# Performance work log

Measured on AMD Instinct MI355X. Metric: run time of the kernel, lower is better.

The kernel has to match this reference:

```python
import jax, jax.numpy as jnp
import numpy as np

VOCAB, E, HIDDEN = 100000, 64, (64, 128, 64)
B, T = 4096, 200


def setup_inputs() -> dict:
    key = jax.random.key(0)
    ks = jax.random.split(key, 12)
    # glorot-ish scales
    def glorot(k, shape):
        fan_in, fan_out = shape[0], shape[-1]
        s = jnp.sqrt(6.0 / (fan_in + fan_out))
        return jax.random.uniform(k, shape, jnp.float32, -s, s)
    return {
        "query": jax.random.randint(ks[0], (B,), 0, VOCAB),
        "keys": jax.random.randint(ks[1], (B, T), 0, VOCAB),
        "emb": glorot(ks[2], (VOCAB, E)),
        "att_w1": glorot(ks[3], (4 * E, 64)),
        "att_b1": jnp.zeros((64,), jnp.float32),
        "att_w2": glorot(ks[4], (64, 1)),
        "att_b2": jnp.zeros((1,), jnp.float32),
        "deep_w1": glorot(ks[5], (HIDDEN[0], HIDDEN[1])),
        "deep_b1": jnp.zeros((HIDDEN[1],), jnp.float32),
        "deep_w2": glorot(ks[6], (HIDDEN[1], HIDDEN[2])),
        "deep_b2": jnp.zeros((HIDDEN[2],), jnp.float32),
        "out_w": glorot(ks[7], (HIDDEN[2], 1)),
        "out_b": jnp.zeros((1,), jnp.float32),
    }


def reference(query, keys, emb, att_w1, att_b1, att_w2, att_b2,
              deep_w1, deep_b1, deep_w2, deep_b2, out_w, out_b):
    q = emb[query]                # [B, E]
    k = emb[keys]                 # [B, T, E]
    qe = jnp.broadcast_to(q[:, None, :], k.shape)  # [B, T, E]
    inter = jnp.concatenate([qe, k, qe - k, qe * k], axis=-1)  # [B, T, 4E]
    h = jax.nn.relu(inter @ att_w1 + att_b1)       # [B, T, 64]
    scores = (h @ att_w2 + att_b2)[..., 0]         # [B, T]
    w = jax.nn.softmax(scores, axis=-1)            # [B, T]
    interest = jnp.einsum("bt,bte->be", w, k)      # [B, E]
    d = jax.nn.relu(interest @ deep_w1 + deep_b1)
    d = jax.nn.relu(d @ deep_w2 + deep_b2)
    return jax.nn.sigmoid(d @ out_w + out_b)       # [B, 1]
```

## Files before the change

kernel.cpp:

```cpp
#include <hip/hip_runtime.h>

#define T 200
#define E 64
#define TPAD 256
#define ROW 72
#define BDIM 256
#define TP 208

typedef __bf16 bf16_t;
typedef __bf16 bf16x8 __attribute__((ext_vector_type(8)));
typedef float f32x4 __attribute__((ext_vector_type(4)));

__global__ __launch_bounds__(256) void emb_cvt(const float* __restrict__ src,
                                               bf16_t* __restrict__ dst, int n8) {
    const int i = blockIdx.x * 256 + threadIdx.x;
    if (i >= n8) return;
    const float4* s = (const float4*)src + (size_t)i * 2;
    const float4 a = s[0], b = s[1];
    union { bf16_t h[8]; uint4 v; } u;
    u.h[0] = (bf16_t)a.x; u.h[1] = (bf16_t)a.y; u.h[2] = (bf16_t)a.z; u.h[3] = (bf16_t)a.w;
    u.h[4] = (bf16_t)b.x; u.h[5] = (bf16_t)b.y; u.h[6] = (bf16_t)b.z; u.h[7] = (bf16_t)b.w;
    ((uint4*)dst)[i] = u.v;
}

__global__ __launch_bounds__(256) void w1_cvt(const float* __restrict__ w1,
                                              float* __restrict__ Ap,
                                              float* __restrict__ Ctf,
                                              float* __restrict__ Dtf) {
    const int idx = blockIdx.x * 256 + threadIdx.x;
    const int e = idx >> 6, j = idx & 63;
    const float a = w1[e * 64 + j];
    const float b = w1[(64 + e) * 64 + j];
    const float c = w1[(128 + e) * 64 + j];
    const float d = w1[(192 + e) * 64 + j];
    Ap[e * 64 + j]  = a + c;
    Ctf[j * 64 + e] = b - c;
    Dtf[j * 64 + e] = d;
}

__global__ __launch_bounds__(256, 4) void din_fast(
    const int* __restrict__ query,
    const int* __restrict__ keys,
    const bf16_t* __restrict__ emb16,
    const float* __restrict__ Ap,
    const float* __restrict__ Ctf,
    const float* __restrict__ Dtf,
    const float* __restrict__ b1,
    const float* __restrict__ w2,
    const float* __restrict__ b2,
    const float* __restrict__ dw1,
    const float* __restrict__ db1,
    const float* __restrict__ dw2,
    const float* __restrict__ db2,
    const float* __restrict__ ow,
    const float* __restrict__ ob,
    float* __restrict__ out)
{
    __shared__ __align__(16) char smem[39936];
    bf16_t* sK   = (bf16_t*)smem;
    bf16_t* sMt  = (bf16_t*)(smem + 29952);
    float*  sUP  = (float*)(smem + 39168);
    float*  sQf  = (float*)(smem + 39680);
    float*  sWgt = (float*)(smem + 29952);
    float*  sRed = (float*)(smem + 30784);
    float*  sInt = (float*)(smem + 30816);
    float*  sD1  = (float*)(smem + 31072);
    float*  sD2  = (float*)(smem + 31584);
    float*  sIP  = (float*)(smem + 31840);

    const int tid  = threadIdx.x;
    const int lane = tid & 63;
    const int wid  = tid >> 6;
    const int b    = blockIdx.x;
    const float b2v = b2[0];

    uint4 kr[8];
    if (tid < T) {
        const int ki = keys[b * T + tid];
        const uint4* kp = (const uint4*)(emb16 + (size_t)ki * E);
        #pragma unroll
        for (int c = 0; c < 8; ++c) kr[c] = kp[c];
    } else {
        #pragma unroll
        for (int c = 0; c < 8; ++c) kr[c] = make_uint4(0u, 0u, 0u, 0u);
    }

    const int qi = query[b];
    if (tid < 64) sQf[tid] = (float)emb16[(size_t)qi * E + tid];
    __syncthreads();

    if (tid < 128) {
        const int j = tid & 63, ec = tid >> 6;
        float au = 0.f;
        #pragma unroll
        for (int eo = 0; eo < 32; ++eo) {
            const int e = ec * 32 + eo;
            au = fmaf(sQf[e], Ap[e * 64 + j], au);
        }
        sUP[tid] = au;
    }
    {
        const int j = tid & 63, h = tid >> 6;
        const float* cp = Ctf + j * 64 + h * 16;
        const float* dp = Dtf + j * 64 + h * 16;
        const float* qp = sQf + h * 16;
        bf16_t mo[16] __attribute__((aligned(16)));
        #pragma unroll
        for (int x = 0; x < 16; ++x)
            mo[x] = (bf16_t)fmaf(qp[x], dp[x], cp[x]);
        *(bf16x8*)&sMt[j * ROW + h * 16]     = *(bf16x8*)&mo[0];
        *(bf16x8*)&sMt[j * ROW + h * 16 + 8] = *(bf16x8*)&mo[8];
    }
    __syncthreads();

    if (tid < TP) {
        uint4* dst = (uint4*)(sK + tid * ROW);
        #pragma unroll
        for (int c = 0; c < 8; ++c) dst[c] = kr[c];
    }
    __syncthreads();

    {
        const int n    = lane & 15;
        const int quad = lane >> 4;
        float w2v[4], uv[4];
        bf16x8 bF[4][2];
        #pragma unroll
        for (int nt = 0; nt < 4; ++nt) {
            const int jj = nt * 16 + n;
            w2v[nt] = w2[jj];
            uv[nt]  = b1[jj] + sUP[jj] + sUP[64 + jj];
            bF[nt][0] = *(const bf16x8*)&sMt[jj * ROW + quad * 8];
            bF[nt][1] = *(const bf16x8*)&sMt[jj * ROW + 32 + quad * 8];
        }
        __syncthreads();

        for (int mt = wid; mt < 13; mt += 4) {
            const bf16x8 a0 = *(const bf16x8*)&sK[(mt * 16 + n) * ROW + quad * 8];
            const bf16x8 a1 = *(const bf16x8*)&sK[(mt * 16 + n) * ROW + 32 + quad * 8];
            float s0 = 0.f, s1 = 0.f, s2 = 0.f, s3 = 0.f;
            #pragma unroll
            for (int nt = 0; nt < 4; ++nt) {
                f32x4 acc = { uv[nt], uv[nt], uv[nt], uv[nt] };
                acc = __builtin_amdgcn_mfma_f32_16x16x32_bf16(a0, bF[nt][0], acc, 0, 0, 0);
                acc = __builtin_amdgcn_mfma_f32_16x16x32_bf16(a1, bF[nt][1], acc, 0, 0, 0);
                s0 = fmaf(fmaxf(acc[0], 0.f), w2v[nt], s0);
                s1 = fmaf(fmaxf(acc[1], 0.f), w2v[nt], s1);
                s2 = fmaf(fmaxf(acc[2], 0.f), w2v[nt], s2);
                s3 = fmaf(fmaxf(acc[3], 0.f), w2v[nt], s3);
            }
            #pragma unroll
            for (int off = 1; off < 16; off <<= 1) {
                s0 += __shfl_xor(s0, off);
                s1 += __shfl_xor(s1, off);
                s2 += __shfl_xor(s2, off);
                s3 += __shfl_xor(s3, off);
            }
            if (n == 0) {
                const int base = mt * 16 + quad * 4;
                sWgt[base + 0] = s0;
                sWgt[base + 1] = s1;
                sWgt[base + 2] = s2;
                sWgt[base + 3] = s3;
            }
        }
    }
    __syncthreads();

    {
        const float score = (tid < T) ? (sWgt[tid] + b2v) : -1e30f;
        float m = score;
        #pragma unroll
        for (int off = 32; off > 0; off >>= 1) m = fmaxf(m, __shfl_xor(m, off));
        if (lane == 0) sRed[wid] = m;
        __syncthreads();
        const float gmax = fmaxf(fmaxf(sRed[0], sRed[1]), fmaxf(sRed[2], sRed[3]));
        const float p = (tid < T) ? __expf(score - gmax) : 0.f;
        float s = p;
        #pragma unroll
        for (int off = 32; off > 0; off >>= 1) s += __shfl_xor(s, off);
        if (lane == 0) sRed[4 + wid] = s;
        __syncthreads();
        const float gsum = sRed[4] + sRed[5] + sRed[6] + sRed[7];
        if (tid < T) sWgt[tid] = p / gsum;
    }
    __syncthreads();

    {
        const int e = tid & 63, ch = tid >> 6;
        float a = 0.f;
        #pragma unroll 10
        for (int tt = 0; tt < 50; ++tt) {
            const int t = ch * 50 + tt;
            a = fmaf(sWgt[t], (float)sK[t * ROW + e], a);
        }
        sIP[tid] = a;
    }
    __syncthreads();
    if (tid < 64) sInt[tid] = sIP[tid] + sIP[64 + tid] + sIP[128 + tid] + sIP[192 + tid];
    __syncthreads();

    if (tid < 128) {
        float a = db1[tid];
        #pragma unroll 8
        for (int e = 0; e < 64; ++e) a = fmaf(sInt[e], dw1[e * 128 + tid], a);
        sD1[tid] = fmaxf(a, 0.f);
    }
    __syncthreads();
    if (tid < 64) {
        float a = db2[tid];
        #pragma unroll 8
        for (int i = 0; i < 128; ++i) a = fmaf(sD1[i], dw2[i * 64 + tid], a);
        sD2[tid] = fmaxf(a, 0.f);
    }
    __syncthreads();
    if (tid < 64) {
        float v = sD2[tid] * ow[tid];
        #pragma unroll
        for (int off = 32; off > 0; off >>= 1) v += __shfl_xor(v, off);
        if (tid == 0) out[b] = 1.f / (1.f + __expf(-(v + ob[0])));
    }
}

__global__ __launch_bounds__(BDIM, 3) void din_kernel(
    const int* __restrict__ query,
    const int* __restrict__ keys,
    const float* __restrict__ embf,
    const bf16_t* __restrict__ emb16,
    const int use16,
    const float* __restrict__ w1,
    const float* __restrict__ b1,
    const float* __restrict__ w2,
    const float* __restrict__ b2,
    const float* __restrict__ dw1,
    const float* __restrict__ db1,
    const float* __restrict__ dw2,
    const float* __restrict__ db2,
    const float* __restrict__ ow,
    const float* __restrict__ ob,
    float* __restrict__ out)
{
    __shared__ __align__(16) char sRaw[TPAD * ROW * 2];
    __shared__ __align__(16) bf16_t sMt[64 * ROW];
    __shared__ float sU[64];
    __shared__ float sUP[256];
    __shared__ float sW2f[64];
    __shared__ float sWgt[256];
    __shared__ float sQf[64];
    __shared__ __align__(16) char sQtmp[128];
    __shared__ float sRed[8];
    __shared__ float sInt[64];
    __shared__ float sD1[128];
    __shared__ float sD2[64];

    const int tid  = threadIdx.x;
    const int lane = tid & 63;
    const int wid  = tid >> 6;
    const int b    = blockIdx.x;
    const float b2v = b2[0];

    uint4 kr[8];
    if (tid < T) {
        const int ki = keys[b * T + tid];
        if (use16) {
            const uint4* kp = (const uint4*)(emb16 + (size_t)ki * E);
            #pragma unroll
            for (int c = 0; c < 8; ++c) kr[c] = kp[c];
        } else {
            const float4* kp = (const float4*)(embf + (size_t)ki * E);
            #pragma unroll
            for (int c = 0; c < 8; ++c) {
                const float4 x = kp[2 * c], y = kp[2 * c + 1];
                union { bf16_t h[8]; uint4 v; } u;
                u.h[0] = (bf16_t)x.x; u.h[1] = (bf16_t)x.y; u.h[2] = (bf16_t)x.z; u.h[3] = (bf16_t)x.w;
                u.h[4] = (bf16_t)y.x; u.h[5] = (bf16_t)y.y; u.h[6] = (bf16_t)y.z; u.h[7] = (bf16_t)y.w;
                kr[c] = u.v;
            }
        }
    } else {
        #pragma unroll
        for (int c = 0; c < 8; ++c) kr[c] = make_uint4(0u, 0u, 0u, 0u);
    }

    const int qi = query[b];
    if (tid < 8) {
        uint4 qv;
        if (use16) {
            qv = ((const uint4*)(emb16 + (size_t)qi * E))[tid];
        } else {
            const float4 x = ((const float4*)(embf + (size_t)qi * E))[2 * tid];
            const float4 y = ((const float4*)(embf + (size_t)qi * E))[2 * tid + 1];
            union { bf16_t h[8]; uint4 v; } u;
            u.h[0] = (bf16_t)x.x; u.h[1] = (bf16_t)x.y; u.h[2] = (bf16_t)x.z; u.h[3] = (bf16_t)x.w;
            u.h[4] = (bf16_t)y.x; u.h[5] = (bf16_t)y.y; u.h[6] = (bf16_t)y.z; u.h[7] = (bf16_t)y.w;
            qv = u.v;
        }
        ((uint4*)sQtmp)[tid] = qv;
    }
    if (tid < 64) sW2f[tid] = w2[tid];
    __syncthreads();
    if (tid < 64) sQf[tid] = (float)((const bf16_t*)sQtmp)[tid];
    __syncthreads();

    {
        float* sTmp = (float*)sRaw;
        const int j = tid & 63, ec = tid >> 6;
        float au = 0.f;
        #pragma unroll
        for (int eo = 0; eo < 16; ++eo) {
            const int e = ec * 16 + eo;
            const float w1a = w1[e * 64 + j];
            const float w1b = w1[(64 + e) * 64 + j];
            const float w1c = w1[(128 + e) * 64 + j];
            const float w1d = w1[(192 + e) * 64 + j];
            sTmp[e * 65 + j] = w1b - w1c + sQf[e] * w1d;
            au = fmaf(sQf[e], w1a + w1c, au);
        }
        sUP[tid] = au;
    }
    __syncthreads();
    {
        const float* sTmp = (const float*)sRaw;
        const int e = tid & 63, jc = tid >> 6;
        #pragma unroll
        for (int jo = 0; jo < 16; ++jo) {
            const int j = jc * 16 + jo;
            sMt[j * ROW + e] = (bf16_t)sTmp[e * 65 + j];
        }
    }
    if (tid < 64) sU[tid] = b1[tid] + sUP[tid] + sUP[64 + tid] + sUP[128 + tid] + sUP[192 + tid];
    __syncthreads();

    bf16_t* sK = (bf16_t*)sRaw;
    {
        uint4* dst = (uint4*)(sK + tid * ROW);
        #pragma unroll
        for (int c = 0; c < 8; ++c) dst[c] = kr[c];
    }
    __syncthreads();

    {
        const int n    = lane & 15;
        const int quad = lane >> 4;
        float w2v[4], uv[4];
        bf16x8 bF[4][2];
        #pragma unroll
        for (int nt = 0; nt < 4; ++nt) {
            w2v[nt] = sW2f[nt * 16 + n];
            uv[nt]  = sU[nt * 16 + n];
            bF[nt][0] = *(const bf16x8*)&sMt[(nt * 16 + n) * ROW + quad * 8];
            bF[nt][1] = *(const bf16x8*)&sMt[(nt * 16 + n) * ROW + 32 + quad * 8];
        }
        #pragma unroll
        for (int i = 0; i < 4; ++i) {
            const int mt = wid * 4 + i;
            const bf16x8 a0 = *(const bf16x8*)&sK[(mt * 16 + n) * ROW + quad * 8];
            const bf16x8 a1 = *(const bf16x8*)&sK[(mt * 16 + n) * ROW + 32 + quad * 8];
            float s0 = 0.f, s1 = 0.f, s2 = 0.f, s3 = 0.f;
            #pragma unroll
            for (int nt = 0; nt < 4; ++nt) {
                f32x4 acc = { uv[nt], uv[nt], uv[nt], uv[nt] };
                acc = __builtin_amdgcn_mfma_f32_16x16x32_bf16(a0, bF[nt][0], acc, 0, 0, 0);
                acc = __builtin_amdgcn_mfma_f32_16x16x32_bf16(a1, bF[nt][1], acc, 0, 0, 0);
                s0 = fmaf(fmaxf(acc[0], 0.f), w2v[nt], s0);
                s1 = fmaf(fmaxf(acc[1], 0.f), w2v[nt], s1);
                s2 = fmaf(fmaxf(acc[2], 0.f), w2v[nt], s2);
                s3 = fmaf(fmaxf(acc[3], 0.f), w2v[nt], s3);
            }
            #pragma unroll
            for (int off = 1; off < 16; off <<= 1) {
                s0 += __shfl_xor(s0, off);
                s1 += __shfl_xor(s1, off);
                s2 += __shfl_xor(s2, off);
                s3 += __shfl_xor(s3, off);
            }
            if (n == 0) {
                const int base = mt * 16 + quad * 4;
                sWgt[base + 0] = s0;
                sWgt[base + 1] = s1;
                sWgt[base + 2] = s2;
                sWgt[base + 3] = s3;
            }
        }
    }
    __syncthreads();

    {
        const float score = (tid < T) ? (sWgt[tid] + b2v) : -1e30f;
        float m = score;
        #pragma unroll
        for (int off = 32; off > 0; off >>= 1) m = fmaxf(m, __shfl_xor(m, off));
        if (lane == 0) sRed[wid] = m;
        __syncthreads();
        const float gmax = fmaxf(fmaxf(sRed[0], sRed[1]), fmaxf(sRed[2], sRed[3]));
        const float p = (tid < T) ? __expf(score - gmax) : 0.f;
        float s = p;
        #pragma unroll
        for (int off = 32; off > 0; off >>= 1) s += __shfl_xor(s, off);
        if (lane == 0) sRed[4 + wid] = s;
        __syncthreads();
        const float gsum = sRed[4] + sRed[5] + sRed[6] + sRed[7];
        sWgt[tid] = p / gsum;
    }
    __syncthreads();

    {
        const int e = tid & 63, ch = tid >> 6;
        float a = 0.f;
        #pragma unroll 8
        for (int tt = 0; tt < 64; ++tt) {
            const int t = ch * 64 + tt;
            a = fmaf(sWgt[t], (float)sK[t * ROW + e], a);
        }
        sUP[tid] = a;
    }
    __syncthreads();
    if (tid < 64) sInt[tid] = sUP[tid] + sUP[64 + tid] + sUP[128 + tid] + sUP[192 + tid];
    __syncthreads();

    if (tid < 128) {
        float a = db1[tid];
        #pragma unroll 8
        for (int e = 0; e < 64; ++e) a = fmaf(sInt[e], dw1[e * 128 + tid], a);
        sD1[tid] = fmaxf(a, 0.f);
    }
    __syncthreads();
    if (tid < 64) {
        float a = db2[tid];
        #pragma unroll 8
        for (int i = 0; i < 128; ++i) a = fmaf(sD1[i], dw2[i * 64 + tid], a);
        sD2[tid] = fmaxf(a, 0.f);
    }
    __syncthreads();
    if (tid < 64) {
        float v = sD2[tid] * ow[tid];
        #pragma unroll
        for (int off = 32; off > 0; off >>= 1) v += __shfl_xor(v, off);
        if (tid == 0) out[b] = 1.f / (1.f + __expf(-(v + ob[0])));
    }
}

extern "C" void kernel_launch(void* const* d_in, const int* in_sizes, int n_in,
                              void* d_out, int out_size, void* d_ws, size_t ws_size,
                              hipStream_t stream) {
    const int*   query = (const int*)d_in[0];
    const int*   keys  = (const int*)d_in[1];
    const float* embf  = (const float*)d_in[2];
    const float* w1    = (const float*)d_in[3];
    const float* b1    = (const float*)d_in[4];
    const float* w2    = (const float*)d_in[5];
    const float* b2    = (const float*)d_in[6];
    const float* dw1   = (const float*)d_in[7];
    const float* db1   = (const float*)d_in[8];
    const float* dw2   = (const float*)d_in[9];
    const float* db2   = (const float*)d_in[10];
    const float* ow    = (const float*)d_in[11];
    const float* ob    = (const float*)d_in[12];
    float* out = (float*)d_out;
    const int B        = in_sizes[0];
    const int embElems = in_sizes[2];
    const size_t WOFF  = 49152;

    if (ws_size >= WOFF + (size_t)embElems * 2) {
        float*  Ap    = (float*)d_ws;
        float*  Ctf   = (float*)((char*)d_ws + 16384);
        float*  Dtf   = (float*)((char*)d_ws + 32768);
        bf16_t* emb16 = (bf16_t*)((char*)d_ws + WOFF);
        const int n8 = embElems / 8;
        w1_cvt<<<16, 256, 0, stream>>>(w1, Ap, Ctf, Dtf);
        emb_cvt<<<(n8 + 255) / 256, 256, 0, stream>>>(embf, emb16, n8);
        din_fast<<<B, BDIM, 0, stream>>>(query, keys, emb16, Ap, Ctf, Dtf,
                                         b1, w2, b2, dw1, db1, dw2, db2, ow, ob, out);
    } else {
        const int use16 = (ws_size >= (size_t)embElems * 2) ? 1 : 0;
        bf16_t* emb16 = (bf16_t*)d_ws;
        if (use16) {
            const int n8 = embElems / 8;
            emb_cvt<<<(n8 + 255) / 256, 256, 0, stream>>>(embf, emb16, n8);
        }
        din_kernel<<<B, BDIM, 0, stream>>>(query, keys, embf, emb16, use16,
                                           w1, b1, w2, b2, dw1, db1, dw2, db2, ow, ob, out);
    }
}
```

Baseline: 163.4 us.

## Shrink LDS with XOR-swizzled unpadded rows to raise occupancy to six blocks

Replaces the padded 72-element row layout with 128-byte rows using an XOR swizzle to avoid bank conflicts. The M matrix and the key tile now share the same region, reusing buffers so LDS drops from about 39.9KB to 27.2KB. Launch bounds go from 4 to 6 blocks per CU. The weighted-sum stage uses 128 threads over 100 timesteps each, which removes one reduction barrier. The swizzled layout leaves padded rows 200-207 uninitialised for the 13th MFMA tile; those scores are masked later, but the register cap of 6 blocks per CU may cause spills.

```diff
diff --git a/kernel.cpp b/kernel.cpp
--- a/kernel.cpp
+++ b/kernel.cpp
@@ -5,7 +5,6 @@
 #define TPAD 256
 #define ROW 72
 #define BDIM 256
-#define TP 208
 
 typedef __bf16 bf16_t;
 typedef __bf16 bf16x8 __attribute__((ext_vector_type(8)));
@@ -38,7 +37,7 @@
     Dtf[j * 64 + e] = d;
 }
 
-__global__ __launch_bounds__(256, 4) void din_fast(
+__global__ __launch_bounds__(256, 6) void din_fast(
     const int* __restrict__ query,
     const int* __restrict__ keys,
     const bf16_t* __restrict__ emb16,
@@ -56,17 +55,14 @@
     const float* __restrict__ ob,
     float* __restrict__ out)
 {
-    __shared__ __align__(16) char smem[39936];
-    bf16_t* sK   = (bf16_t*)smem;
-    bf16_t* sMt  = (bf16_t*)(smem + 29952);
-    float*  sUP  = (float*)(smem + 39168);
-    float*  sQf  = (float*)(smem + 39680);
-    float*  sWgt = (float*)(smem + 29952);
-    float*  sRed = (float*)(smem + 30784);
-    float*  sInt = (float*)(smem + 30816);
-    float*  sD1  = (float*)(smem + 31072);
-    float*  sD2  = (float*)(smem + 31584);
-    float*  sIP  = (float*)(smem + 31840);
+    __shared__ __align__(16) char smem[27232];
+    float* sWgt = (float*)(smem + 25600);
+    float* sRed = (float*)(smem + 26432);
+    float* sIP  = (float*)(smem + 26464);
+    float* sQf  = (float*)(smem + 26976);
+    float* sUP  = (float*)(smem + 25600);
+    float* sD1  = (float*)(smem + 25600);
+    float* sD2  = (float*)(smem + 26112);
 
     const int tid  = threadIdx.x;
     const int lane = tid & 63;
@@ -80,27 +76,25 @@
         const uint4* kp = (const uint4*)(emb16 + (size_t)ki * E);
         #pragma unroll
         for (int c = 0; c < 8; ++c) kr[c] = kp[c];
-    } else {
-        #pragma unroll
-        for (int c = 0; c < 8; ++c) kr[c] = make_uint4(0u, 0u, 0u, 0u);
     }
 
     const int qi = query[b];
     if (tid < 64) sQf[tid] = (float)emb16[(size_t)qi * E + tid];
     __syncthreads();
 
+    const int j = tid & 63;
+    const int h = tid >> 6;
+
     if (tid < 128) {
-        const int j = tid & 63, ec = tid >> 6;
         float au = 0.f;
         #pragma unroll
         for (int eo = 0; eo < 32; ++eo) {
-            const int e = ec * 32 + eo;
+            const int e = h * 32 + eo;
             au = fmaf(sQf[e], Ap[e * 64 + j], au);
         }
         sUP[tid] = au;
     }
     {
-        const int j = tid & 63, h = tid >> 6;
         const float* cp = Ctf + j * 64 + h * 16;
         const float* dp = Dtf + j * 64 + h * 16;
         const float* qp = sQf + h * 16;
@@ -108,36 +102,44 @@
         #pragma unroll
         for (int x = 0; x < 16; ++x)
             mo[x] = (bf16_t)fmaf(qp[x], dp[x], cp[x]);
-        *(bf16x8*)&sMt[j * ROW + h * 16]     = *(bf16x8*)&mo[0];
-        *(bf16x8*)&sMt[j * ROW + h * 16 + 8] = *(bf16x8*)&mo[8];
-    }
-    __syncthreads();
-
-    if (tid < TP) {
-        uint4* dst = (uint4*)(sK + tid * ROW);
-        #pragma unroll
-        for (int c = 0; c < 8; ++c) dst[c] = kr[c];
-    }
-    __syncthreads();
-
-    {
-        const int n    = lane & 15;
-        const int quad = lane >> 4;
-        float w2v[4], uv[4];
-        bf16x8 bF[4][2];
-        #pragma unroll
-        for (int nt = 0; nt < 4; ++nt) {
-            const int jj = nt * 16 + n;
-            w2v[nt] = w2[jj];
-            uv[nt]  = b1[jj] + sUP[jj] + sUP[64 + jj];
-            bF[nt][0] = *(const bf16x8*)&sMt[jj * ROW + quad * 8];
-            bF[nt][1] = *(const bf16x8*)&sMt[jj * ROW + 32 + quad * 8];
-        }
-        __syncthreads();
-
+        char* rowp = smem + j * 128;
+        const int rx = (j & 7) << 4;
+        *(uint4*)(rowp + ((h * 32) ^ rx))      = *(uint4*)&mo[0];
+        *(uint4*)(rowp + ((h * 32 + 16) ^ rx)) = *(uint4*)&mo[8];
+    }
+    __syncthreads();
+
+    const int n    = lane & 15;
+    const int quad = lane >> 4;
+    float w2v[4], uv[4];
+    bf16x8 bF[4][2];
+    #pragma unroll
+    for (int nt = 0; nt < 4; ++nt) {
+        const int jj = nt * 16 + n;
+        w2v[nt] = w2[jj];
+        uv[nt]  = b1[jj] + sUP[jj] + sUP[64 + jj];
+        const char* rp = smem + jj * 128;
+        const int rxj = (jj & 7) << 4;
+        bF[nt][0] = *(const bf16x8*)(rp + ((quad * 16) ^ rxj));
+        bF[nt][1] = *(const bf16x8*)(rp + ((64 + quad * 16) ^ rxj));
+    }
+    __syncthreads();
+
+    if (tid < T) {
+        char* rowp = smem + tid * 128;
+        const int rx = (tid & 7) << 4;
+        #pragma unroll
+        for (int c = 0; c < 8; ++c)
+            *(uint4*)(rowp + ((c * 16) ^ rx)) = kr[c];
+    }
+    __syncthreads();
+
+    {
+        const int rxn = (n & 7) << 4;
         for (int mt = wid; mt < 13; mt += 4) {
-            const bf16x8 a0 = *(const bf16x8*)&sK[(mt * 16 + n) * ROW + quad * 8];
-            const bf16x8 a1 = *(const bf16x8*)&sK[(mt * 16 + n) * ROW + 32 + quad * 8];
+            const char* rp = smem + (mt * 16 + n) * 128;
+            const bf16x8 a0 = *(const bf16x8*)(rp + ((quad * 16) ^ rxn));
+            const bf16x8 a1 = *(const bf16x8*)(rp + ((64 + quad * 16) ^ rxn));
             float s0 = 0.f, s1 = 0.f, s2 = 0.f, s3 = 0.f;
             #pragma unroll
             for (int nt = 0; nt < 4; ++nt) {
@@ -186,24 +188,24 @@
     }
     __syncthreads();
 
-    {
+    if (tid < 128) {
         const int e = tid & 63, ch = tid >> 6;
         float a = 0.f;
         #pragma unroll 10
-        for (int tt = 0; tt < 50; ++tt) {
-            const int t = ch * 50 + tt;
-            a = fmaf(sWgt[t], (float)sK[t * ROW + e], a);
+        for (int tt = 0; tt < 100; ++tt) {
+            const int t = ch * 100 + tt;
+            const bf16_t kv = *(const bf16_t*)(smem + t * 128 + ((e * 2) ^ ((t & 7) << 4)));
+            a = fmaf(sWgt[t], (float)kv, a);
         }
         sIP[tid] = a;
     }
-    __syncthreads();
-    if (tid < 64) sInt[tid] = sIP[tid] + sIP[64 + tid] + sIP[128 + tid] + sIP[192 + tid];
     __syncthreads();
 
     if (tid < 128) {
         float a = db1[tid];
         #pragma unroll 8
-        for (int e = 0; e < 64; ++e) a = fmaf(sInt[e], dw1[e * 128 + tid], a);
+        for (int e = 0; e < 64; ++e)
+            a = fmaf(sIP[e] + sIP[64 + e], dw1[e * 128 + tid], a);
         sD1[tid] = fmaxf(a, 0.f);
     }
     __syncthreads();
```

Measured after the change: 220.1 us. 1.35x slower.

## Merge preprocessing kernels and coalesce key-embedding gather across 8-thread groups

Applied to the files above, without the earlier changes.

Merges the weight-transform and embedding-conversion kernels into one launch, saving one kernel launch and the gap between launches. Changes the key-row gather so each group of 8 threads loads one 128-byte embedding row with each thread taking one 16-byte chunk, instead of one thread loading a whole row. This should give coalesced global loads and fewer outstanding loads per thread. The fallback path no longer builds a bf16 copy and always uses the fp32 embedding table.

```diff
diff --git a/kernel.cpp b/kernel.cpp
--- a/kernel.cpp
+++ b/kernel.cpp
@@ -11,31 +11,33 @@
 typedef __bf16 bf16x8 __attribute__((ext_vector_type(8)));
 typedef float f32x4 __attribute__((ext_vector_type(4)));
 
-__global__ __launch_bounds__(256) void emb_cvt(const float* __restrict__ src,
-                                               bf16_t* __restrict__ dst, int n8) {
-    const int i = blockIdx.x * 256 + threadIdx.x;
+__global__ __launch_bounds__(256) void pre_cvt(const float* __restrict__ embf,
+                                               bf16_t* __restrict__ emb16, int n8,
+                                               const float* __restrict__ w1,
+                                               float* __restrict__ Ap,
+                                               float* __restrict__ Ctf,
+                                               float* __restrict__ Dtf) {
+    const int bid = blockIdx.x;
+    if (bid < 16) {
+        const int idx = bid * 256 + threadIdx.x;
+        const int e = idx >> 6, j = idx & 63;
+        const float a = w1[e * 64 + j];
+        const float b = w1[(64 + e) * 64 + j];
+        const float c = w1[(128 + e) * 64 + j];
+        const float d = w1[(192 + e) * 64 + j];
+        Ap[e * 64 + j]  = a + c;
+        Ctf[j * 64 + e] = b - c;
+        Dtf[j * 64 + e] = d;
+        return;
+    }
+    const int i = (bid - 16) * 256 + threadIdx.x;
     if (i >= n8) return;
-    const float4* s = (const float4*)src + (size_t)i * 2;
+    const float4* s = (const float4*)embf + (size_t)i * 2;
     const float4 a = s[0], b = s[1];
     union { bf16_t h[8]; uint4 v; } u;
     u.h[0] = (bf16_t)a.x; u.h[1] = (bf16_t)a.y; u.h[2] = (bf16_t)a.z; u.h[3] = (bf16_t)a.w;
     u.h[4] = (bf16_t)b.x; u.h[5] = (bf16_t)b.y; u.h[6] = (bf16_t)b.z; u.h[7] = (bf16_t)b.w;
-    ((uint4*)dst)[i] = u.v;
-}
-
-__global__ __launch_bounds__(256) void w1_cvt(const float* __restrict__ w1,
-                                              float* __restrict__ Ap,
-                                              float* __restrict__ Ctf,
-                                              float* __restrict__ Dtf) {
-    const int idx = blockIdx.x * 256 + threadIdx.x;
-    const int e = idx >> 6, j = idx & 63;
-    const float a = w1[e * 64 + j];
-    const float b = w1[(64 + e) * 64 + j];
-    const float c = w1[(128 + e) * 64 + j];
-    const float d = w1[(192 + e) * 64 + j];
-    Ap[e * 64 + j]  = a + c;
-    Ctf[j * 64 + e] = b - c;
-    Dtf[j * 64 + e] = d;
+    ((uint4*)emb16)[i] = u.v;
 }
 
 __global__ __launch_bounds__(256, 4) void din_fast(
@@ -74,15 +76,18 @@
     const int b    = blockIdx.x;
     const float b2v = b2[0];
 
-    uint4 kr[8];
-    if (tid < T) {
-        const int ki = keys[b * T + tid];
-        const uint4* kp = (const uint4*)(emb16 + (size_t)ki * E);
-        #pragma unroll
-        for (int c = 0; c < 8; ++c) kr[c] = kp[c];
-    } else {
-        #pragma unroll
-        for (int c = 0; c < 8; ++c) kr[c] = make_uint4(0u, 0u, 0u, 0u);
+    const int c8    = tid & 7;
+    const int rbase = tid >> 3;
+    uint4 kr[7];
+    #pragma unroll
+    for (int i = 0; i < 7; ++i) {
+        const int t = rbase + 32 * i;
+        if (t < T) {
+            const int ki = keys[b * T + t];
+            kr[i] = ((const uint4*)(emb16 + (size_t)ki * E))[c8];
+        } else {
+            kr[i] = make_uint4(0u, 0u, 0u, 0u);
+        }
     }
 
     const int qi = query[b];
@@ -113,10 +118,10 @@
     }
     __syncthreads();
 
-    if (tid < TP) {
-        uint4* dst = (uint4*)(sK + tid * ROW);
-        #pragma unroll
-        for (int c = 0; c < 8; ++c) dst[c] = kr[c];
+    #pragma unroll
+    for (int i = 0; i < 7; ++i) {
+        const int t = rbase + 32 * i;
+        if (t < TP) *(uint4*)&sK[t * ROW + c8 * 8] = kr[i];
     }
     __syncthreads();
 
@@ -467,18 +472,12 @@
         float*  Dtf   = (float*)((char*)d_ws + 32768);
         bf16_t* emb16 = (bf16_t*)((char*)d_ws + WOFF);
         const int n8 = embElems / 8;
-        w1_cvt<<<16, 256, 0, stream>>>(w1, Ap, Ctf, Dtf);
-        emb_cvt<<<(n8 + 255) / 256, 256, 0, stream>>>(embf, emb16, n8);
+        pre_cvt<<<16 + (n8 + 255) / 256, 256, 0, stream>>>(embf, emb16, n8,
+                                                           w1, Ap, Ctf, Dtf);
         din_fast<<<B, BDIM, 0, stream>>>(query, keys, emb16, Ap, Ctf, Dtf,
                                          b1, w2, b2, dw1, db1, dw2, db2, ow, ob, out);
     } else {
-        const int use16 = (ws_size >= (size_t)embElems * 2) ? 1 : 0;
-        bf16_t* emb16 = (bf16_t*)d_ws;
-        if (use16) {
-            const int n8 = embElems / 8;
-            emb_cvt<<<(n8 + 255) / 256, 256, 0, stream>>>(embf, emb16, n8);
-        }
-        din_kernel<<<B, BDIM, 0, stream>>>(query, keys, embf, emb16, use16,
+        din_kernel<<<B, BDIM, 0, stream>>>(query, keys, embf, (const bf16_t*)d_ws, 0,
                                            w1, b1, w2, b2, dw1, db1, dw2, db2, ow, ob, out);
     }
 }
```

After: 167.1 us. +2.3%, slower.
